# Performance work log

Hardware: AMD Instinct MI355X
Metric: run time of the kernel (lower is better)

The kernel has to match this reference:

```python
import jax, jax.numpy as jnp
import numpy as np

TWO_PI = 2.0 * np.pi


def setup_inputs() -> dict:
    key = jax.random.key(0)
    ks = jax.random.split(key, 6)
    n1 = n2 = n3 = 20
    nk, ni, nspin = 4, 16, 2
    # Invertible, physically plausible lattice (~8 Bohr cubic cell + jitter)
    A = jnp.eye(3, dtype=jnp.float32) * 8.0 + 0.05 * jax.random.normal(ks[0], (3, 3), jnp.float32)
    k_grid = 0.1 * jax.random.normal(ks[1], (nk, 3), jnp.float32)
    cg_real = jax.random.normal(ks[2], (nspin, nk, ni, n1, n2, n3), jnp.float32)
    cg_imag = jax.random.normal(ks[3], (nspin, nk, ni, n1, n2, n3), jnp.float32)
    # Real-space evaluation grid: fractional coords in [0,1)^3 mapped through A
    frac = jax.random.uniform(ks[4], (n1, n2, n3, 3), jnp.float32)
    r = frac @ A
    return {"A": A, "k_grid": k_grid, "cg_real": cg_real, "cg_imag": cg_imag, "r": r}


def reference(A, k_grid, cg_real, cg_imag, r):
    # cg: [spin, nk, ni, n1, n2, n3] complex plane-wave coefficients
    cg = cg_real + 1j * cg_imag
    n1, n2, n3 = cg.shape[-3:]
    # Integer FFT frequency mesh m -> reciprocal-lattice vectors G = m @ B,
    # B rows are reciprocal basis: B = 2*pi * inv(A)^T  (A rows = lattice vecs)
    f1 = jnp.fft.fftfreq(n1) * n1
    f2 = jnp.fft.fftfreq(n2) * n2
    f3 = jnp.fft.fftfreq(n3) * n3
    m = jnp.stack(jnp.meshgrid(f1, f2, f3, indexing="ij"), axis=-1).astype(A.dtype)  # [n1,n2,n3,3]
    B = TWO_PI * jnp.linalg.inv(A).T
    G = (m @ B).reshape(-1, 3)                      # [nG, 3]
    vol = jnp.abs(jnp.linalg.det(A))
    Rf = r.reshape(-1, 3)                           # [nR, 3]
    # Plane-wave synthesis: psi_{s,k,i}(r) = exp(i k.r)/sqrt(vol) * sum_G c_G exp(i G.r)
    # (equivalent to the triple-nested vmap over the grid dims, fully vectorized)
    phase_g = jnp.exp(1j * (Rf @ G.T))              # [nR, nG] complex
    dens = cg.reshape(*cg.shape[:3], -1)            # [spin, nk, ni, nG]
    psi = jnp.einsum("skin,rn->skir", dens, phase_g)  # [spin, nk, ni, nR]
    phase_k = jnp.exp(1j * (Rf @ k_grid.T))         # [nR, nk]
    psi = psi * jnp.moveaxis(phase_k, 0, -1)[None, :, None, :]
    psi = psi / jnp.sqrt(vol).astype(psi.real.dtype)
    # [spin, nk, ni, n1, n2, n3] -- matches moveaxis(range(3), range(-3,0))
    return psi.reshape(*cg.shape[:3], *r.shape[:-1])
```

## Files before the change

### kernel.cpp

```cpp
#include <hip/hip_runtime.h>

typedef __attribute__((ext_vector_type(4))) float f32x4;
typedef __attribute__((ext_vector_type(8))) short s16x8;

#define NG     8000
#define NRPT   8000
#define NSKIN  128
#define MT     128
#define NT     64
#define KK     32
#define KCH    800
#define NKC    10
#define NTILES 25
#define NRB    125
#define TPB    256
#define WS_TILE_B 16384
#define WS_NEED   ((size_t)NKC*NTILES*WS_TILE_B)

#define S_AR 0
#define S_AI 8192
#define S_BC 16384
#define S_BS 20480
#define S_SZ 24576

__device__ __forceinline__ float sin_rev(float u){ float r; asm("v_sin_f32 %0, %1" : "=v"(r) : "v"(u)); return r; }
__device__ __forceinline__ float cos_rev(float u){ float r; asm("v_cos_f32 %0, %1" : "=v"(r) : "v"(u)); return r; }
__device__ __forceinline__ unsigned int cvt_pk(float lo, float hi){
    unsigned int r; asm("v_cvt_pk_bf16_f32 %0, %1, %2" : "=v"(r) : "v"(lo), "v"(hi)); return r;
}
__device__ __forceinline__ s16x8 bneg(s16x8 v){
    int4 u = *(int4*)&v;
    u.x ^= 0x80008000; u.y ^= 0x80008000; u.z ^= 0x80008000; u.w ^= 0x80008000;
    return *(s16x8*)&u;
}
__device__ __forceinline__ int swz(int row, int kg){
    return row*64 + ((kg ^ ((row>>1)&3))<<4);
}
__device__ __forceinline__ void glds16(const void* g, void* l){
    __builtin_amdgcn_global_load_lds((const __attribute__((address_space(1))) void*)g,
                                     (__attribute__((address_space(3))) void*)l, 16, 0, 0);
}

__global__ __launch_bounds__(256) void bloch_prepass(
    const float* __restrict__ cgr, const float* __restrict__ cgi,
    char* __restrict__ ws)
{
    int gid = blockIdx.x*256 + threadIdx.x;
    if (gid >= NKC*NTILES*2*512) return;
    int slot  = gid & 3;
    int row   = (gid >> 2) & 127;
    int pt    = gid >> 9;
    int plane = pt & 1;
    int tileIdx = pt >> 1;
    int t  = tileIdx % NTILES;
    int kc = tileIdx / NTILES;
    int kg = slot ^ ((row >> 1) & 3);
    int k  = kc*KCH + t*KK + kg*8;
    const float* src = plane ? cgi : cgr;
    const float4 v0 = *(const float4*)&src[(size_t)row*NG + k];
    const float4 v1 = *(const float4*)&src[(size_t)row*NG + k + 4];
    uint4 p;
    p.x = cvt_pk(v0.x, v0.y); p.y = cvt_pk(v0.z, v0.w);
    p.z = cvt_pk(v1.x, v1.y); p.w = cvt_pk(v1.z, v1.w);
    *(uint4*)(ws + (size_t)gid*16) = p;
}

template<bool PRE>
__global__ __launch_bounds__(TPB, 4) void bloch8(
    const float* __restrict__ Amat, const float* __restrict__ kgrid,
    const float* __restrict__ cgr,  const float* __restrict__ cgi,
    const float* __restrict__ rpts, const char* __restrict__ ws,
    float* __restrict__ out, int out_size)
{
    __shared__ __align__(16) char smem[S_SZ];
    __shared__ float fracS[NT][4];
    __shared__ float invAS[9];
    __shared__ float scaleS;

    const int tid = threadIdx.x;
    const int bid = blockIdx.x;
    const int kc  = bid >> 7;
    const int rb  = bid & 127;
    if (rb >= NRB) return;
    const int r_base  = rb * NT;
    const int k_begin = kc * KCH;

    if (tid == 0) {
        float a00=Amat[0],a01=Amat[1],a02=Amat[2];
        float a10=Amat[3],a11=Amat[4],a12=Amat[5];
        float a20=Amat[6],a21=Amat[7],a22=Amat[8];
        float c00 =  (a11*a22 - a12*a21);
        float c01 = -(a10*a22 - a12*a20);
        float c02 =  (a10*a21 - a11*a20);
        float det = a00*c00 + a01*c01 + a02*c02;
        float id  = 1.0f/det;
        invAS[0] =  c00*id;
        invAS[1] = -(a01*a22 - a02*a21)*id;
        invAS[2] =  (a01*a12 - a02*a11)*id;
        invAS[3] =  c01*id;
        invAS[4] =  (a00*a22 - a02*a20)*id;
        invAS[5] = -(a00*a12 - a02*a10)*id;
        invAS[6] =  c02*id;
        invAS[7] = -(a00*a21 - a01*a20)*id;
        invAS[8] =  (a00*a11 - a01*a10)*id;
        scaleS   = rsqrtf(fabsf(det));
    }
    __syncthreads();

    if (tid < NT) {
        int rg = r_base + tid;
        float r0 = rpts[rg*3+0], r1 = rpts[rg*3+1], r2 = rpts[rg*3+2];
        fracS[tid][0] = r0*invAS[0] + r1*invAS[3] + r2*invAS[6];
        fracS[tid][1] = r0*invAS[1] + r1*invAS[4] + r2*invAS[7];
        fracS[tid][2] = r0*invAS[2] + r1*invAS[5] + r2*invAS[8];
    }
    __syncthreads();

    f32x4 accRe[4][2], accIm[4][2];
    #pragma unroll
    for (int mi = 0; mi < 4; ++mi)
        #pragma unroll
        for (int ni = 0; ni < 2; ++ni) {
            accRe[mi][ni] = (f32x4){0.f,0.f,0.f,0.f};
            accIm[mi][ni] = (f32x4){0.f,0.f,0.f,0.f};
        }

    const int lane = tid & 63;
    const int wid  = tid >> 6;
    const int wm   = wid >> 1;
    const int wn   = wid & 1;
    const int frow = lane & 15;
    const int kq   = lane >> 4;

    const int sB   = tid >> 2;
    const int qtr  = tid & 3;
    const int stOffB = swz(sB, qtr);
    const int aOff   = swz(wm*64 + frow, kq);
    const int bOff   = swz(wn*32 + frow, kq);

    const float f0r = fracS[sB][0], f1r = fracS[sB][1], f2r = fracS[sB][2];

    float u1 = f2r - floorf(f2r);
    const float w1c = cos_rev(u1), w1s = sin_rev(u1);
    float yd = -20.0f * f2r; yd -= floorf(yd);
    const float wdc = cos_rev(yd), wds = sin_rev(yd);
    const float w1wdc = w1c*wdc - w1s*wds;
    const float w1wds = w1c*wds + w1s*wdc;

    #pragma unroll 1
    for (int t = 0; t < NTILES; ++t) {
        const int kb = k_begin + t*KK;

        if (PRE) {
            const char* tb = ws + (size_t)(kc*NTILES + t)*WS_TILE_B;
            glds16(tb +         tid*16,        smem + S_AR +        tid*16);
            glds16(tb + 4096 +  tid*16,        smem + S_AR + 4096 + tid*16);
            glds16(tb + 8192 +  tid*16,        smem + S_AI +        tid*16);
            glds16(tb + 12288 + tid*16,        smem + S_AI + 4096 + tid*16);
        } else {
            #pragma unroll
            for (int j = 0; j < 2; ++j) {
                int row = (tid>>2) + 64*j;
                int kg  = qtr ^ ((row>>1)&3);
                int k   = kb + kg*8;
                const float4 v0r = *(const float4*)&cgr[(size_t)row*NG + k];
                const float4 v1r = *(const float4*)&cgr[(size_t)row*NG + k + 4];
                const float4 v0i = *(const float4*)&cgi[(size_t)row*NG + k];
                const float4 v1i = *(const float4*)&cgi[(size_t)row*NG + k + 4];
                uint4 pr, pi;
                pr.x = cvt_pk(v0r.x, v0r.y); pr.y = cvt_pk(v0r.z, v0r.w);
                pr.z = cvt_pk(v1r.x, v1r.y); pr.w = cvt_pk(v1r.z, v1r.w);
                pi.x = cvt_pk(v0i.x, v0i.y); pi.y = cvt_pk(v0i.z, v0i.w);
                pi.z = cvt_pk(v1i.x, v1i.y); pi.w = cvt_pk(v1i.z, v1i.w);
                *(uint4*)(smem + S_AR + row*64 + qtr*16) = pr;
                *(uint4*)(smem + S_AI + row*64 + qtr*16) = pi;
            }
        }

        {
            int g0   = kb + qtr*8;
            int i12  = (g0 * 3277) >> 16;
            int i3_0 = g0 - i12*20;
            int i1a  = (i12 * 3277) >> 16; int i2a = i12 - i1a*20;
            int i12b = i12 + 1;
            int i1b  = (i12b * 3277) >> 16; int i2b = i12b - i1b*20;
            float m1a = (float)(i1a - (i1a >= 10 ? 20 : 0));
            float m2a = (float)(i2a - (i2a >= 10 ? 20 : 0));
            float m1b = (float)(i1b - (i1b >= 10 ? 20 : 0));
            float m2b = (float)(i2b - (i2b >= 10 ? 20 : 0));
            float m30 = (float)(i3_0 - (i3_0 >= 10 ? 20 : 0));
            float y0 = m1a*f0r + m2a*f1r + m30*f2r; y0 -= floorf(y0);
            float cc = cos_rev(y0), cs = sin_rev(y0);
            float rd = (m1b-m1a)*f0r + (m2b-m2a)*f1r; rd -= floorf(rd);
            float rc = cos_rev(rd), rs = sin_rev(rd);
            float wXc = w1c*rc - w1s*rs;
            float wXs = w1c*rs + w1s*rc;
            float bcv[8], bsv[8];
            bcv[0] = cc; bsv[0] = cs;
            #pragma unroll
            for (int j = 1; j < 8; ++j) {
                bool cB = (i3_0 == 20 - j);
                bool cD = (i3_0 == 10 - j);
                float mc = cB ? wXc : (cD ? w1wdc : w1c);
                float ms = cB ? wXs : (cD ? w1wds : w1s);
                float nc = cc*mc - cs*ms;
                float ns = cc*ms + cs*mc;
                cc = nc; cs = ns;
                bcv[j] = cc; bsv[j] = cs;
            }
            uint4 wc, wsn;
            wc.x  = cvt_pk(bcv[0], bcv[1]); wc.y  = cvt_pk(bcv[2], bcv[3]);
            wc.z  = cvt_pk(bcv[4], bcv[5]); wc.w  = cvt_pk(bcv[6], bcv[7]);
            wsn.x = cvt_pk(bsv[0], bsv[1]); wsn.y = cvt_pk(bsv[2], bsv[3]);
            wsn.z = cvt_pk(bsv[4], bsv[5]); wsn.w = cvt_pk(bsv[6], bsv[7]);
            *(uint4*)(smem + S_BC + stOffB) = wc;
            *(uint4*)(smem + S_BS + stOffB) = wsn;
        }
        __syncthreads();

        s16x8 bcf[2], bsf[2], bsnf[2];
        #pragma unroll
        for (int ni = 0; ni < 2; ++ni) {
            bcf[ni]  = *(const s16x8*)(smem + S_BC + bOff + ni*1024);
            bsf[ni]  = *(const s16x8*)(smem + S_BS + bOff + ni*1024);
            bsnf[ni] = bneg(bsf[ni]);
        }
        #pragma unroll
        for (int mi = 0; mi < 4; ++mi) {
            s16x8 arf = *(const s16x8*)(smem + S_AR + aOff + mi*1024);
            s16x8 aif = *(const s16x8*)(smem + S_AI + aOff + mi*1024);
            #pragma unroll
            for (int ni = 0; ni < 2; ++ni) {
                accRe[mi][ni] = __builtin_amdgcn_mfma_f32_16x16x32_bf16(arf, bcf[ni],  accRe[mi][ni], 0, 0, 0);
                accRe[mi][ni] = __builtin_amdgcn_mfma_f32_16x16x32_bf16(aif, bsnf[ni], accRe[mi][ni], 0, 0, 0);
                accIm[mi][ni] = __builtin_amdgcn_mfma_f32_16x16x32_bf16(arf, bsf[ni],  accIm[mi][ni], 0, 0, 0);
                accIm[mi][ni] = __builtin_amdgcn_mfma_f32_16x16x32_bf16(aif, bcf[ni],  accIm[mi][ni], 0, 0, 0);
            }
        }
        __syncthreads();
    }

    float2* ekr = (float2*)smem;
    {
        int col = tid >> 2, kidx = tid & 3;
        int rg = r_base + col;
        float r0 = rpts[rg*3+0], r1 = rpts[rg*3+1], r2 = rpts[rg*3+2];
        float ang = (r0*kgrid[kidx*3+0] + r1*kgrid[kidx*3+1] + r2*kgrid[kidx*3+2])
                    * 0.15915494309189535f;
        float u = ang - floorf(ang);
        ekr[col*4+kidx] = make_float2(cos_rev(u), sin_rev(u));
    }
    __syncthreads();

    const bool write_imag = (out_size >= 2*NSKIN*NRPT);
    const float scale = scaleS;
    #pragma unroll
    for (int mi = 0; mi < 4; ++mi) {
        const int m0 = wm*64 + mi*16;
        const int kidx = (m0 >> 4) & 3;
        #pragma unroll
        for (int ni = 0; ni < 2; ++ni) {
            int col = wn*32 + ni*16 + frow;
            int rg = r_base + col;
            float2 e = ekr[col*4+kidx];
            float ck = e.x, sk = e.y;
            #pragma unroll
            for (int v = 0; v < 4; ++v) {
                int sg = m0 + kq*4 + v;
                float re = accRe[mi][ni][v];
                float im = accIm[mi][ni][v];
                float orr = (re*ck - im*sk) * scale;
                size_t lin = (size_t)sg * NRPT + rg;
                if (write_imag) {
                    float oi = (re*sk + im*ck) * scale;
                    size_t idx = lin * 2;
                    if (idx + 1 < (size_t)out_size) {
                        atomicAdd(&out[idx],   orr);
                        atomicAdd(&out[idx+1], oi);
                    }
                } else {
                    atomicAdd(&out[lin], orr);
                }
            }
        }
    }
}

extern "C" void kernel_launch(void* const* d_in, const int* in_sizes, int n_in,
                              void* d_out, int out_size, void* d_ws, size_t ws_size,
                              hipStream_t stream) {
    const float* Amat  = (const float*)d_in[0];
    const float* kgrid = (const float*)d_in[1];
    const float* cgr   = (const float*)d_in[2];
    const float* cgi   = (const float*)d_in[3];
    const float* rpts  = (const float*)d_in[4];
    float* out = (float*)d_out;

    hipMemsetAsync(d_out, 0, (size_t)out_size * sizeof(float), stream);

    const bool use_pre = (ws_size >= WS_NEED);
    dim3 grid(NKC * 128);
    if (use_pre) {
        bloch_prepass<<<dim3(NKC*NTILES*2*512/256), 256, 0, stream>>>(cgr, cgi, (char*)d_ws);
        bloch8<true><<<grid, TPB, 0, stream>>>(Amat, kgrid, cgr, cgi, rpts,
                                               (const char*)d_ws, out, out_size);
    } else {
        bloch8<false><<<grid, TPB, 0, stream>>>(Amat, kgrid, cgr, cgi, rpts,
                                                nullptr, out, out_size);
    }
}
```

Measured before the change: 88.56 us.

## Use three-multiply complex GEMM and halve point tile width

Replaces the four real MFMA products per complex tile with a Karatsuba-style three-product scheme, precomputing bf16 Ar+Ai and cos+sin planes and recombining real/imag parts in the epilogue. The point tile shrinks from 64 to 32, doubling the grid, with only half the threads generating phase factors. This cuts matrix-core work but increases A-tile traffic per point and adds bf16 rounding error from the summed operands.

```diff
diff --git a/kernel.cpp b/kernel.cpp
--- a/kernel.cpp
+++ b/kernel.cpp
@@ -6,32 +6,28 @@
 #define NG     8000
 #define NRPT   8000
 #define NSKIN  128
-#define MT     128
-#define NT     64
+#define NT     32
 #define KK     32
 #define KCH    800
 #define NKC    10
 #define NTILES 25
-#define NRB    125
+#define NTOT   (NKC*NTILES)
 #define TPB    256
-#define WS_TILE_B 16384
-#define WS_NEED   ((size_t)NKC*NTILES*WS_TILE_B)
+#define WS_TILE_B 24576
+#define WS_NEED   ((size_t)NTOT*WS_TILE_B)
 
 #define S_AR 0
 #define S_AI 8192
-#define S_BC 16384
-#define S_BS 20480
-#define S_SZ 24576
+#define S_AS 16384
+#define S_BC 24576
+#define S_BS 26624
+#define S_BU 28672
+#define S_SZ 30720
 
 __device__ __forceinline__ float sin_rev(float u){ float r; asm("v_sin_f32 %0, %1" : "=v"(r) : "v"(u)); return r; }
 __device__ __forceinline__ float cos_rev(float u){ float r; asm("v_cos_f32 %0, %1" : "=v"(r) : "v"(u)); return r; }
 __device__ __forceinline__ unsigned int cvt_pk(float lo, float hi){
     unsigned int r; asm("v_cvt_pk_bf16_f32 %0, %1, %2" : "=v"(r) : "v"(lo), "v"(hi)); return r;
-}
-__device__ __forceinline__ s16x8 bneg(s16x8 v){
-    int4 u = *(int4*)&v;
-    u.x ^= 0x80008000; u.y ^= 0x80008000; u.z ^= 0x80008000; u.w ^= 0x80008000;
-    return *(s16x8*)&u;
 }
 __device__ __forceinline__ int swz(int row, int kg){
     return row*64 + ((kg ^ ((row>>1)&3))<<4);
@@ -46,27 +42,34 @@
     char* __restrict__ ws)
 {
     int gid = blockIdx.x*256 + threadIdx.x;
-    if (gid >= NKC*NTILES*2*512) return;
+    if (gid >= NTOT*3*512) return;
     int slot  = gid & 3;
     int row   = (gid >> 2) & 127;
     int pt    = gid >> 9;
-    int plane = pt & 1;
-    int tileIdx = pt >> 1;
-    int t  = tileIdx % NTILES;
-    int kc = tileIdx / NTILES;
+    int tileIdx = pt / 3;
+    int plane   = pt - tileIdx*3;
     int kg = slot ^ ((row >> 1) & 3);
-    int k  = kc*KCH + t*KK + kg*8;
-    const float* src = plane ? cgi : cgr;
-    const float4 v0 = *(const float4*)&src[(size_t)row*NG + k];
-    const float4 v1 = *(const float4*)&src[(size_t)row*NG + k + 4];
+    int k  = tileIdx*KK + kg*8;
     uint4 p;
-    p.x = cvt_pk(v0.x, v0.y); p.y = cvt_pk(v0.z, v0.w);
-    p.z = cvt_pk(v1.x, v1.y); p.w = cvt_pk(v1.z, v1.w);
+    if (plane == 0 || plane == 1) {
+        const float* src = plane ? cgi : cgr;
+        const float4 v0 = *(const float4*)&src[(size_t)row*NG + k];
+        const float4 v1 = *(const float4*)&src[(size_t)row*NG + k + 4];
+        p.x = cvt_pk(v0.x, v0.y); p.y = cvt_pk(v0.z, v0.w);
+        p.z = cvt_pk(v1.x, v1.y); p.w = cvt_pk(v1.z, v1.w);
+    } else {
+        const float4 r0 = *(const float4*)&cgr[(size_t)row*NG + k];
+        const float4 r1 = *(const float4*)&cgr[(size_t)row*NG + k + 4];
+        const float4 i0 = *(const float4*)&cgi[(size_t)row*NG + k];
+        const float4 i1 = *(const float4*)&cgi[(size_t)row*NG + k + 4];
+        p.x = cvt_pk(r0.x+i0.x, r0.y+i0.y); p.y = cvt_pk(r0.z+i0.z, r0.w+i0.w);
+        p.z = cvt_pk(r1.x+i1.x, r1.y+i1.y); p.w = cvt_pk(r1.z+i1.z, r1.w+i1.w);
+    }
     *(uint4*)(ws + (size_t)gid*16) = p;
 }
 
 template<bool PRE>
-__global__ __launch_bounds__(TPB, 4) void bloch8(
+__global__ __launch_bounds__(TPB, 4) void bloch9(
     const float* __restrict__ Amat, const float* __restrict__ kgrid,
     const float* __restrict__ cgr,  const float* __restrict__ cgi,
     const float* __restrict__ rpts, const char* __restrict__ ws,
@@ -79,9 +82,9 @@
 
     const int tid = threadIdx.x;
     const int bid = blockIdx.x;
-    const int kc  = bid >> 7;
-    const int rb  = bid & 127;
-    if (rb >= NRB) return;
+    const int kc  = bid >> 8;
+    const int rb  = bid & 255;
+    if (rb >= 250) return;
     const int r_base  = rb * NT;
     const int k_begin = kc * KCH;
 
@@ -116,14 +119,13 @@
     }
     __syncthreads();
 
-    f32x4 accRe[4][2], accIm[4][2];
+    f32x4 accP1[4], accP2[4], accP3[4];
     #pragma unroll
-    for (int mi = 0; mi < 4; ++mi)
-        #pragma unroll
-        for (int ni = 0; ni < 2; ++ni) {
-            accRe[mi][ni] = (f32x4){0.f,0.f,0.f,0.f};
-            accIm[mi][ni] = (f32x4){0.f,0.f,0.f,0.f};
-        }
+    for (int mi = 0; mi < 4; ++mi) {
+        accP1[mi] = (f32x4){0.f,0.f,0.f,0.f};
+        accP2[mi] = (f32x4){0.f,0.f,0.f,0.f};
+        accP3[mi] = (f32x4){0.f,0.f,0.f,0.f};
+    }
 
     const int lane = tid & 63;
     const int wid  = tid >> 6;
@@ -132,20 +134,24 @@
     const int frow = lane & 15;
     const int kq   = lane >> 4;
 
-    const int sB   = tid >> 2;
-    const int qtr  = tid & 3;
-    const int stOffB = swz(sB, qtr);
-    const int aOff   = swz(wm*64 + frow, kq);
-    const int bOff   = swz(wn*32 + frow, kq);
-
-    const float f0r = fracS[sB][0], f1r = fracS[sB][1], f2r = fracS[sB][2];
-
-    float u1 = f2r - floorf(f2r);
-    const float w1c = cos_rev(u1), w1s = sin_rev(u1);
-    float yd = -20.0f * f2r; yd -= floorf(yd);
-    const float wdc = cos_rev(yd), wds = sin_rev(yd);
-    const float w1wdc = w1c*wdc - w1s*wds;
-    const float w1wds = w1c*wds + w1s*wdc;
+    const int aOff = swz(wm*64 + frow, kq);
+    const int bOff = swz(wn*16 + frow, kq);
+
+    const int sB  = tid >> 2;
+    const int qtr = tid & 3;
+    const int stOffB = swz(sB & 31, qtr);
+
+    float f0r=0.f, f1r=0.f, f2r=0.f;
+    float w1c=0.f, w1s=0.f, w1wdc=0.f, w1wds=0.f;
+    if (tid < 128) {
+        f0r = fracS[sB][0]; f1r = fracS[sB][1]; f2r = fracS[sB][2];
+        float u1 = f2r - floorf(f2r);
+        w1c = cos_rev(u1); w1s = sin_rev(u1);
+        float yd = -20.0f * f2r; yd -= floorf(yd);
+        float wdc = cos_rev(yd), wds = sin_rev(yd);
+        w1wdc = w1c*wdc - w1s*wds;
+        w1wds = w1c*wds + w1s*wdc;
+    }
 
     #pragma unroll 1
     for (int t = 0; t < NTILES; ++t) {
@@ -153,10 +159,12 @@
 
         if (PRE) {
             const char* tb = ws + (size_t)(kc*NTILES + t)*WS_TILE_B;
-            glds16(tb +         tid*16,        smem + S_AR +        tid*16);
-            glds16(tb + 4096 +  tid*16,        smem + S_AR + 4096 + tid*16);
-            glds16(tb + 8192 +  tid*16,        smem + S_AI +        tid*16);
-            glds16(tb + 12288 + tid*16,        smem + S_AI + 4096 + tid*16);
+            glds16(tb +          tid*16, smem + S_AR +        tid*16);
+            glds16(tb + 4096  +  tid*16, smem + S_AR + 4096 + tid*16);
+            glds16(tb + 8192  +  tid*16, smem + S_AI +        tid*16);
+            glds16(tb + 12288 +  tid*16, smem + S_AI + 4096 + tid*16);
+            glds16(tb + 16384 +  tid*16, smem + S_AS +        tid*16);
+            glds16(tb + 20480 +  tid*16, smem + S_AS + 4096 + tid*16);
         } else {
             #pragma unroll
             for (int j = 0; j < 2; ++j) {
@@ -167,17 +175,20 @@
                 const float4 v1r = *(const float4*)&cgr[(size_t)row*NG + k + 4];
                 const float4 v0i = *(const float4*)&cgi[(size_t)row*NG + k];
                 const float4 v1i = *(const float4*)&cgi[(size_t)row*NG + k + 4];
-                uint4 pr, pi;
+                uint4 pr, pi, ps;
                 pr.x = cvt_pk(v0r.x, v0r.y); pr.y = cvt_pk(v0r.z, v0r.w);
                 pr.z = cvt_pk(v1r.x, v1r.y); pr.w = cvt_pk(v1r.z, v1r.w);
                 pi.x = cvt_pk(v0i.x, v0i.y); pi.y = cvt_pk(v0i.z, v0i.w);
                 pi.z = cvt_pk(v1i.x, v1i.y); pi.w = cvt_pk(v1i.z, v1i.w);
+                ps.x = cvt_pk(v0r.x+v0i.x, v0r.y+v0i.y); ps.y = cvt_pk(v0r.z+v0i.z, v0r.w+v0i.w);
+                ps.z = cvt_pk(v1r.x+v1i.x, v1r.y+v1i.y); ps.w = cvt_pk(v1r.z+v1i.z, v1r.w+v1i.w);
                 *(uint4*)(smem + S_AR + row*64 + qtr*16) = pr;
                 *(uint4*)(smem + S_AI + row*64 + qtr*16) = pi;
-            }
-        }
-
-        {
+                *(uint4*)(smem + S_AS + row*64 + qtr*16) = ps;
+            }
+        }
+
+        if (tid < 128) {
             int g0   = kb + qtr*8;
             int i12  = (g0 * 3277) >> 16;
             int i3_0 = g0 - i12*20;
@@ -208,40 +219,52 @@
                 cc = nc; cs = ns;
                 bcv[j] = cc; bsv[j] = cs;
             }
-            uint4 wc, wsn;
+            uint4 wc, wsn, wu;
             wc.x  = cvt_pk(bcv[0], bcv[1]); wc.y  = cvt_pk(bcv[2], bcv[3]);
             wc.z  = cvt_pk(bcv[4], bcv[5]); wc.w  = cvt_pk(bcv[6], bcv[7]);
             wsn.x = cvt_pk(bsv[0], bsv[1]); wsn.y = cvt_pk(bsv[2], bsv[3]);
             wsn.z = cvt_pk(bsv[4], bsv[5]); wsn.w = cvt_pk(bsv[6], bsv[7]);
+            wu.x  = cvt_pk(bcv[0]+bsv[0], bcv[1]+bsv[1]);
+            wu.y  = cvt_pk(bcv[2]+bsv[2], bcv[3]+bsv[3]);
+            wu.z  = cvt_pk(bcv[4]+bsv[4], bcv[5]+bsv[5]);
+            wu.w  = cvt_pk(bcv[6]+bsv[6], bcv[7]+bsv[7]);
             *(uint4*)(smem + S_BC + stOffB) = wc;
             *(uint4*)(smem + S_BS + stOffB) = wsn;
+            *(uint4*)(smem + S_BU + stOffB) = wu;
         }
         __syncthreads();
 
-        s16x8 bcf[2], bsf[2], bsnf[2];
-        #pragma unroll
-        for (int ni = 0; ni < 2; ++ni) {
-            bcf[ni]  = *(const s16x8*)(smem + S_BC + bOff + ni*1024);
-            bsf[ni]  = *(const s16x8*)(smem + S_BS + bOff + ni*1024);
-            bsnf[ni] = bneg(bsf[ni]);
-        }
-        #pragma unroll
-        for (int mi = 0; mi < 4; ++mi) {
-            s16x8 arf = *(const s16x8*)(smem + S_AR + aOff + mi*1024);
-            s16x8 aif = *(const s16x8*)(smem + S_AI + aOff + mi*1024);
-            #pragma unroll
-            for (int ni = 0; ni < 2; ++ni) {
-                accRe[mi][ni] = __builtin_amdgcn_mfma_f32_16x16x32_bf16(arf, bcf[ni],  accRe[mi][ni], 0, 0, 0);
-                accRe[mi][ni] = __builtin_amdgcn_mfma_f32_16x16x32_bf16(aif, bsnf[ni], accRe[mi][ni], 0, 0, 0);
-                accIm[mi][ni] = __builtin_amdgcn_mfma_f32_16x16x32_bf16(arf, bsf[ni],  accIm[mi][ni], 0, 0, 0);
-                accIm[mi][ni] = __builtin_amdgcn_mfma_f32_16x16x32_bf16(aif, bcf[ni],  accIm[mi][ni], 0, 0, 0);
-            }
-        }
+        __builtin_amdgcn_s_setprio(1);
+        {
+            s16x8 b = *(const s16x8*)(smem + S_BC + bOff);
+            #pragma unroll
+            for (int mi = 0; mi < 4; ++mi) {
+                s16x8 a = *(const s16x8*)(smem + S_AR + aOff + mi*1024);
+                accP1[mi] = __builtin_amdgcn_mfma_f32_16x16x32_bf16(a, b, accP1[mi], 0, 0, 0);
+            }
+        }
+        {
+            s16x8 b = *(const s16x8*)(smem + S_BS + bOff);
+            #pragma unroll
+            for (int mi = 0; mi < 4; ++mi) {
+                s16x8 a = *(const s16x8*)(smem + S_AI + aOff + mi*1024);
+                accP2[mi] = __builtin_amdgcn_mfma_f32_16x16x32_bf16(a, b, accP2[mi], 0, 0, 0);
+            }
+        }
+        {
+            s16x8 b = *(const s16x8*)(smem + S_BU + bOff);
+            #pragma unroll
+            for (int mi = 0; mi < 4; ++mi) {
+                s16x8 a = *(const s16x8*)(smem + S_AS + aOff + mi*1024);
+                accP3[mi] = __builtin_amdgcn_mfma_f32_16x16x32_bf16(a, b, accP3[mi], 0, 0, 0);
+            }
+        }
+        __builtin_amdgcn_s_setprio(0);
         __syncthreads();
     }
 
     float2* ekr = (float2*)smem;
-    {
+    if (tid < 128) {
         int col = tid >> 2, kidx = tid & 3;
         int rg = r_base + col;
         float r0 = rpts[rg*3+0], r1 = rpts[rg*3+1], r2 = rpts[rg*3+2];
@@ -254,33 +277,30 @@
 
     const bool write_imag = (out_size >= 2*NSKIN*NRPT);
     const float scale = scaleS;
+    const int col = wn*16 + frow;
+    const int rg  = r_base + col;
     #pragma unroll
     for (int mi = 0; mi < 4; ++mi) {
         const int m0 = wm*64 + mi*16;
-        const int kidx = (m0 >> 4) & 3;
+        float2 e = ekr[col*4 + mi];
+        float ck = e.x, sk = e.y;
         #pragma unroll
-        for (int ni = 0; ni < 2; ++ni) {
-            int col = wn*32 + ni*16 + frow;
-            int rg = r_base + col;
-            float2 e = ekr[col*4+kidx];
-            float ck = e.x, sk = e.y;
-            #pragma unroll
-            for (int v = 0; v < 4; ++v) {
-                int sg = m0 + kq*4 + v;
-                float re = accRe[mi][ni][v];
-                float im = accIm[mi][ni][v];
-                float orr = (re*ck - im*sk) * scale;
-                size_t lin = (size_t)sg * NRPT + rg;
-                if (write_imag) {
-                    float oi = (re*sk + im*ck) * scale;
-                    size_t idx = lin * 2;
-                    if (idx + 1 < (size_t)out_size) {
-                        atomicAdd(&out[idx],   orr);
-                        atomicAdd(&out[idx+1], oi);
-                    }
-                } else {
-                    atomicAdd(&out[lin], orr);
+        for (int v = 0; v < 4; ++v) {
+            int sg = m0 + kq*4 + v;
+            float p1 = accP1[mi][v], p2 = accP2[mi][v], p3 = accP3[mi][v];
+            float re = p1 - p2;
+            float im = p3 - p1 - p2;
+            float orr = (re*ck - im*sk) * scale;
+            size_t lin = (size_t)sg * NRPT + rg;
+            if (write_imag) {
+                float oi = (re*sk + im*ck) * scale;
+                size_t idx = lin * 2;
+                if (idx + 1 < (size_t)out_size) {
+                    atomicAdd(&out[idx],   orr);
+                    atomicAdd(&out[idx+1], oi);
                 }
+            } else {
+                atomicAdd(&out[lin], orr);
             }
         }
     }
@@ -299,13 +319,13 @@
     hipMemsetAsync(d_out, 0, (size_t)out_size * sizeof(float), stream);
 
     const bool use_pre = (ws_size >= WS_NEED);
-    dim3 grid(NKC * 128);
+    dim3 grid(NKC * 256);
     if (use_pre) {
-        bloch_prepass<<<dim3(NKC*NTILES*2*512/256), 256, 0, stream>>>(cgr, cgi, (char*)d_ws);
-        bloch8<true><<<grid, TPB, 0, stream>>>(Amat, kgrid, cgr, cgi, rpts,
+        bloch_prepass<<<dim3(NTOT*3*512/256), 256, 0, stream>>>(cgr, cgi, (char*)d_ws);
+        bloch9<true><<<grid, TPB, 0, stream>>>(Amat, kgrid, cgr, cgi, rpts,
                                                (const char*)d_ws, out, out_size);
     } else {
-        bloch8<false><<<grid, TPB, 0, stream>>>(Amat, kgrid, cgr, cgi, rpts,
+        bloch9<false><<<grid, TPB, 0, stream>>>(Amat, kgrid, cgr, cgi, rpts,
                                                 nullptr, out, out_size);
     }
 }
```

New measurement: 104.9 us. 1.18x slower.

## Load A fragments directly from prepacked global and double-buffer phase tiles

Applied to the files above, without the earlier changes.

The prepass now lays out bf16 coefficients in MFMA fragment order, so each wave loads its A operands straight from global into registers instead of staging them through LDS. The phase-factor (B) tile is double-buffered in LDS, and the next tile is generated while the current MFMAs run, leaving one barrier per iteration. MFMA issue is raised with s_setprio. The price is more registers (launch bounds drop to 3 waves/SIMD), so occupancy is lower, and there is no global-load latency hiding beyond what the compiler schedules.

```diff
diff --git a/kernel.cpp b/kernel.cpp
--- a/kernel.cpp
+++ b/kernel.cpp
@@ -6,22 +6,15 @@
 #define NG     8000
 #define NRPT   8000
 #define NSKIN  128
-#define MT     128
 #define NT     64
 #define KK     32
 #define KCH    800
 #define NKC    10
 #define NTILES 25
-#define NRB    125
+#define NTOT   (NKC*NTILES)
 #define TPB    256
 #define WS_TILE_B 16384
-#define WS_NEED   ((size_t)NKC*NTILES*WS_TILE_B)
-
-#define S_AR 0
-#define S_AI 8192
-#define S_BC 16384
-#define S_BS 20480
-#define S_SZ 24576
+#define WS_NEED   ((size_t)NTOT*WS_TILE_B)
 
 __device__ __forceinline__ float sin_rev(float u){ float r; asm("v_sin_f32 %0, %1" : "=v"(r) : "v"(u)); return r; }
 __device__ __forceinline__ float cos_rev(float u){ float r; asm("v_cos_f32 %0, %1" : "=v"(r) : "v"(u)); return r; }
@@ -33,12 +26,14 @@
     u.x ^= 0x80008000; u.y ^= 0x80008000; u.z ^= 0x80008000; u.w ^= 0x80008000;
     return *(s16x8*)&u;
 }
+__device__ __forceinline__ s16x8 pack8(float4 v0, float4 v1){
+    union { s16x8 v; uint4 u; } r;
+    r.u.x = cvt_pk(v0.x,v0.y); r.u.y = cvt_pk(v0.z,v0.w);
+    r.u.z = cvt_pk(v1.x,v1.y); r.u.w = cvt_pk(v1.z,v1.w);
+    return r.v;
+}
 __device__ __forceinline__ int swz(int row, int kg){
     return row*64 + ((kg ^ ((row>>1)&3))<<4);
-}
-__device__ __forceinline__ void glds16(const void* g, void* l){
-    __builtin_amdgcn_global_load_lds((const __attribute__((address_space(1))) void*)g,
-                                     (__attribute__((address_space(3))) void*)l, 16, 0, 0);
 }
 
 __global__ __launch_bounds__(256) void bloch_prepass(
@@ -46,16 +41,13 @@
     char* __restrict__ ws)
 {
     int gid = blockIdx.x*256 + threadIdx.x;
-    if (gid >= NKC*NTILES*2*512) return;
-    int slot  = gid & 3;
-    int row   = (gid >> 2) & 127;
-    int pt    = gid >> 9;
-    int plane = pt & 1;
-    int tileIdx = pt >> 1;
-    int t  = tileIdx % NTILES;
-    int kc = tileIdx / NTILES;
-    int kg = slot ^ ((row >> 1) & 3);
-    int k  = kc*KCH + t*KK + kg*8;
+    if (gid >= NTOT*2*8*64) return;
+    int lane  = gid & 63;
+    int rb8   = (gid >> 6) & 7;
+    int plane = (gid >> 9) & 1;
+    int tile  = gid >> 10;
+    int row   = rb8*16 + (lane & 15);
+    int k     = tile*KK + (lane >> 4)*8;
     const float* src = plane ? cgi : cgr;
     const float4 v0 = *(const float4*)&src[(size_t)row*NG + k];
     const float4 v1 = *(const float4*)&src[(size_t)row*NG + k + 4];
@@ -66,13 +58,13 @@
 }
 
 template<bool PRE>
-__global__ __launch_bounds__(TPB, 4) void bloch8(
+__global__ __launch_bounds__(TPB, 3) void bloch10(
     const float* __restrict__ Amat, const float* __restrict__ kgrid,
     const float* __restrict__ cgr,  const float* __restrict__ cgi,
     const float* __restrict__ rpts, const char* __restrict__ ws,
     float* __restrict__ out, int out_size)
 {
-    __shared__ __align__(16) char smem[S_SZ];
+    __shared__ __align__(16) char smemB[2*8192];
     __shared__ float fracS[NT][4];
     __shared__ float invAS[9];
     __shared__ float scaleS;
@@ -81,7 +73,7 @@
     const int bid = blockIdx.x;
     const int kc  = bid >> 7;
     const int rb  = bid & 127;
-    if (rb >= NRB) return;
+    if (rb >= 125) return;
     const int r_base  = rb * NT;
     const int k_begin = kc * KCH;
 
@@ -135,7 +127,6 @@
     const int sB   = tid >> 2;
     const int qtr  = tid & 3;
     const int stOffB = swz(sB, qtr);
-    const int aOff   = swz(wm*64 + frow, kq);
     const int bOff   = swz(wn*32 + frow, kq);
 
     const float f0r = fracS[sB][0], f1r = fracS[sB][1], f2r = fracS[sB][2];
@@ -147,100 +138,101 @@
     const float w1wdc = w1c*wdc - w1s*wds;
     const float w1wds = w1c*wds + w1s*wdc;
 
+    auto stageB = [&](int kb, char* wb){
+        int g0   = kb + qtr*8;
+        int i12  = (g0 * 3277) >> 16;
+        int i3_0 = g0 - i12*20;
+        int i1a  = (i12 * 3277) >> 16; int i2a = i12 - i1a*20;
+        int i12b = i12 + 1;
+        int i1b  = (i12b * 3277) >> 16; int i2b = i12b - i1b*20;
+        float m1a = (float)(i1a - (i1a >= 10 ? 20 : 0));
+        float m2a = (float)(i2a - (i2a >= 10 ? 20 : 0));
+        float m1b = (float)(i1b - (i1b >= 10 ? 20 : 0));
+        float m2b = (float)(i2b - (i2b >= 10 ? 20 : 0));
+        float m30 = (float)(i3_0 - (i3_0 >= 10 ? 20 : 0));
+        float y0 = m1a*f0r + m2a*f1r + m30*f2r; y0 -= floorf(y0);
+        float cc = cos_rev(y0), cs = sin_rev(y0);
+        float rd = (m1b-m1a)*f0r + (m2b-m2a)*f1r; rd -= floorf(rd);
+        float rc = cos_rev(rd), rs = sin_rev(rd);
+        float wXc = w1c*rc - w1s*rs;
+        float wXs = w1c*rs + w1s*rc;
+        float bcv[8], bsv[8];
+        bcv[0] = cc; bsv[0] = cs;
+        #pragma unroll
+        for (int j = 1; j < 8; ++j) {
+            bool cB = (i3_0 == 20 - j);
+            bool cD = (i3_0 == 10 - j);
+            float mc = cB ? wXc : (cD ? w1wdc : w1c);
+            float ms = cB ? wXs : (cD ? w1wds : w1s);
+            float nc = cc*mc - cs*ms;
+            float ns = cc*ms + cs*mc;
+            cc = nc; cs = ns;
+            bcv[j] = cc; bsv[j] = cs;
+        }
+        uint4 wc, wsn;
+        wc.x  = cvt_pk(bcv[0], bcv[1]); wc.y  = cvt_pk(bcv[2], bcv[3]);
+        wc.z  = cvt_pk(bcv[4], bcv[5]); wc.w  = cvt_pk(bcv[6], bcv[7]);
+        wsn.x = cvt_pk(bsv[0], bsv[1]); wsn.y = cvt_pk(bsv[2], bsv[3]);
+        wsn.z = cvt_pk(bsv[4], bsv[5]); wsn.w = cvt_pk(bsv[6], bsv[7]);
+        *(uint4*)(wb +        stOffB) = wc;
+        *(uint4*)(wb + 4096 + stOffB) = wsn;
+    };
+
+    stageB(k_begin, smemB);
+    __syncthreads();
+
     #pragma unroll 1
     for (int t = 0; t < NTILES; ++t) {
         const int kb = k_begin + t*KK;
-
+        const char* bufP = smemB + (t & 1)*8192;
+        char*       bufQ = smemB + ((t + 1) & 1)*8192;
+
+        s16x8 arf[4], aif[4];
         if (PRE) {
-            const char* tb = ws + (size_t)(kc*NTILES + t)*WS_TILE_B;
-            glds16(tb +         tid*16,        smem + S_AR +        tid*16);
-            glds16(tb + 4096 +  tid*16,        smem + S_AR + 4096 + tid*16);
-            glds16(tb + 8192 +  tid*16,        smem + S_AI +        tid*16);
-            glds16(tb + 12288 + tid*16,        smem + S_AI + 4096 + tid*16);
+            const char* tb = ws + (size_t)(kc*NTILES + t)*WS_TILE_B + lane*16;
+            #pragma unroll
+            for (int mi = 0; mi < 4; ++mi) {
+                arf[mi] = *(const s16x8*)(tb +        (wm*4 + mi)*1024);
+                aif[mi] = *(const s16x8*)(tb + 8192 + (wm*4 + mi)*1024);
+            }
         } else {
             #pragma unroll
-            for (int j = 0; j < 2; ++j) {
-                int row = (tid>>2) + 64*j;
-                int kg  = qtr ^ ((row>>1)&3);
-                int k   = kb + kg*8;
-                const float4 v0r = *(const float4*)&cgr[(size_t)row*NG + k];
-                const float4 v1r = *(const float4*)&cgr[(size_t)row*NG + k + 4];
-                const float4 v0i = *(const float4*)&cgi[(size_t)row*NG + k];
-                const float4 v1i = *(const float4*)&cgi[(size_t)row*NG + k + 4];
-                uint4 pr, pi;
-                pr.x = cvt_pk(v0r.x, v0r.y); pr.y = cvt_pk(v0r.z, v0r.w);
-                pr.z = cvt_pk(v1r.x, v1r.y); pr.w = cvt_pk(v1r.z, v1r.w);
-                pi.x = cvt_pk(v0i.x, v0i.y); pi.y = cvt_pk(v0i.z, v0i.w);
-                pi.z = cvt_pk(v1i.x, v1i.y); pi.w = cvt_pk(v1i.z, v1i.w);
-                *(uint4*)(smem + S_AR + row*64 + qtr*16) = pr;
-                *(uint4*)(smem + S_AI + row*64 + qtr*16) = pi;
+            for (int mi = 0; mi < 4; ++mi) {
+                int row = wm*64 + mi*16 + frow;
+                int k   = kb + kq*8;
+                const float* pr_ = &cgr[(size_t)row*NG + k];
+                const float* pi_ = &cgi[(size_t)row*NG + k];
+                arf[mi] = pack8(*(const float4*)pr_, *(const float4*)(pr_+4));
+                aif[mi] = pack8(*(const float4*)pi_, *(const float4*)(pi_+4));
             }
         }
 
-        {
-            int g0   = kb + qtr*8;
-            int i12  = (g0 * 3277) >> 16;
-            int i3_0 = g0 - i12*20;
-            int i1a  = (i12 * 3277) >> 16; int i2a = i12 - i1a*20;
-            int i12b = i12 + 1;
-            int i1b  = (i12b * 3277) >> 16; int i2b = i12b - i1b*20;
-            float m1a = (float)(i1a - (i1a >= 10 ? 20 : 0));
-            float m2a = (float)(i2a - (i2a >= 10 ? 20 : 0));
-            float m1b = (float)(i1b - (i1b >= 10 ? 20 : 0));
-            float m2b = (float)(i2b - (i2b >= 10 ? 20 : 0));
-            float m30 = (float)(i3_0 - (i3_0 >= 10 ? 20 : 0));
-            float y0 = m1a*f0r + m2a*f1r + m30*f2r; y0 -= floorf(y0);
-            float cc = cos_rev(y0), cs = sin_rev(y0);
-            float rd = (m1b-m1a)*f0r + (m2b-m2a)*f1r; rd -= floorf(rd);
-            float rc = cos_rev(rd), rs = sin_rev(rd);
-            float wXc = w1c*rc - w1s*rs;
-            float wXs = w1c*rs + w1s*rc;
-            float bcv[8], bsv[8];
-            bcv[0] = cc; bsv[0] = cs;
-            #pragma unroll
-            for (int j = 1; j < 8; ++j) {
-                bool cB = (i3_0 == 20 - j);
-                bool cD = (i3_0 == 10 - j);
-                float mc = cB ? wXc : (cD ? w1wdc : w1c);
-                float ms = cB ? wXs : (cD ? w1wds : w1s);
-                float nc = cc*mc - cs*ms;
-                float ns = cc*ms + cs*mc;
-                cc = nc; cs = ns;
-                bcv[j] = cc; bsv[j] = cs;
-            }
-            uint4 wc, wsn;
-            wc.x  = cvt_pk(bcv[0], bcv[1]); wc.y  = cvt_pk(bcv[2], bcv[3]);
-            wc.z  = cvt_pk(bcv[4], bcv[5]); wc.w  = cvt_pk(bcv[6], bcv[7]);
-            wsn.x = cvt_pk(bsv[0], bsv[1]); wsn.y = cvt_pk(bsv[2], bsv[3]);
-            wsn.z = cvt_pk(bsv[4], bsv[5]); wsn.w = cvt_pk(bsv[6], bsv[7]);
-            *(uint4*)(smem + S_BC + stOffB) = wc;
-            *(uint4*)(smem + S_BS + stOffB) = wsn;
-        }
-        __syncthreads();
-
         s16x8 bcf[2], bsf[2], bsnf[2];
         #pragma unroll
         for (int ni = 0; ni < 2; ++ni) {
-            bcf[ni]  = *(const s16x8*)(smem + S_BC + bOff + ni*1024);
-            bsf[ni]  = *(const s16x8*)(smem + S_BS + bOff + ni*1024);
+            bcf[ni]  = *(const s16x8*)(bufP +        bOff + ni*1024);
+            bsf[ni]  = *(const s16x8*)(bufP + 4096 + bOff + ni*1024);
             bsnf[ni] = bneg(bsf[ni]);
         }
-        #pragma unroll
-        for (int mi = 0; mi < 4; ++mi) {
-            s16x8 arf = *(const s16x8*)(smem + S_AR + aOff + mi*1024);
-            s16x8 aif = *(const s16x8*)(smem + S_AI + aOff + mi*1024);
+
+        if (t + 1 < NTILES) stageB(kb + KK, bufQ);
+
+        __builtin_amdgcn_s_setprio(1);
+        #pragma unroll
+        for (int mi = 0; mi < 4; ++mi)
             #pragma unroll
             for (int ni = 0; ni < 2; ++ni) {
-                accRe[mi][ni] = __builtin_amdgcn_mfma_f32_16x16x32_bf16(arf, bcf[ni],  accRe[mi][ni], 0, 0, 0);
-                accRe[mi][ni] = __builtin_amdgcn_mfma_f32_16x16x32_bf16(aif, bsnf[ni], accRe[mi][ni], 0, 0, 0);
-                accIm[mi][ni] = __builtin_amdgcn_mfma_f32_16x16x32_bf16(arf, bsf[ni],  accIm[mi][ni], 0, 0, 0);
-                accIm[mi][ni] = __builtin_amdgcn_mfma_f32_16x16x32_bf16(aif, bcf[ni],  accIm[mi][ni], 0, 0, 0);
+                accRe[mi][ni] = __builtin_amdgcn_mfma_f32_16x16x32_bf16(arf[mi], bcf[ni],  accRe[mi][ni], 0, 0, 0);
+                accRe[mi][ni] = __builtin_amdgcn_mfma_f32_16x16x32_bf16(aif[mi], bsnf[ni], accRe[mi][ni], 0, 0, 0);
+                accIm[mi][ni] = __builtin_amdgcn_mfma_f32_16x16x32_bf16(arf[mi], bsf[ni],  accIm[mi][ni], 0, 0, 0);
+                accIm[mi][ni] = __builtin_amdgcn_mfma_f32_16x16x32_bf16(aif[mi], bcf[ni],  accIm[mi][ni], 0, 0, 0);
             }
-        }
+        __builtin_amdgcn_s_setprio(0);
+
         __syncthreads();
     }
 
-    float2* ekr = (float2*)smem;
+    float2* ekr = (float2*)smemB;
     {
         int col = tid >> 2, kidx = tid & 3;
         int rg = r_base + col;
@@ -301,11 +293,11 @@
     const bool use_pre = (ws_size >= WS_NEED);
     dim3 grid(NKC * 128);
     if (use_pre) {
-        bloch_prepass<<<dim3(NKC*NTILES*2*512/256), 256, 0, stream>>>(cgr, cgi, (char*)d_ws);
-        bloch8<true><<<grid, TPB, 0, stream>>>(Amat, kgrid, cgr, cgi, rpts,
-                                               (const char*)d_ws, out, out_size);
+        bloch_prepass<<<dim3(NTOT*2*8*64/256), 256, 0, stream>>>(cgr, cgi, (char*)d_ws);
+        bloch10<true><<<grid, TPB, 0, stream>>>(Amat, kgrid, cgr, cgi, rpts,
+                                                (const char*)d_ws, out, out_size);
     } else {
-        bloch8<false><<<grid, TPB, 0, stream>>>(Amat, kgrid, cgr, cgi, rpts,
-                                                nullptr, out, out_size);
-    }
-}
+        bloch10<false><<<grid, TPB, 0, stream>>>(Amat, kgrid, cgr, cgi, rpts,
+                                                 nullptr, out, out_size);
+    }
+}
```

Result: slower. 90.62 us (+2.3%).
